# Performance work log

Measured on AMD Instinct MI355X. Metric: run time of the kernel, lower is better.

Reference implementation:

```python
import jax, jax.numpy as jnp
import numpy as np
from jax import lax

B_, L_, D_MODEL = 2, 2048, 1024
H, P, N, G, K, CHUNK = 32, 64, 128, 1, 4, 256
INTER = H * P                 # 2048
CONV_DIM = INTER + 2 * G * N  # 2304
PROJ = INTER + CONV_DIM + H   # 4384: [gate | hidden_B_C | dt]
EPS = 1e-6


def segment_sum(x):
    # x: [..., T] -> [..., T, T]; segsum[i,j] = sum_{k=j+1..i} x[k] for i>=j, else -inf
    T = x.shape[-1]
    xx = jnp.repeat(x[..., None], T, axis=-1)
    xx = jnp.where(jnp.tril(jnp.ones((T, T), bool), -1), xx, 0.0)
    s = jnp.cumsum(xx, axis=-2)
    return jnp.where(jnp.tril(jnp.ones((T, T), bool)), s, -jnp.inf)


def setup_inputs() -> dict:
    key = jax.random.key(0)
    ks = jax.random.split(key, 6)
    s = 0.02
    return {
        "x": jax.random.normal(ks[0], (B_, L_, D_MODEL), jnp.float32),
        "in_proj_w": jax.random.normal(ks[1], (PROJ, D_MODEL), jnp.float32) * s,
        "conv_w": jax.random.normal(ks[2], (CONV_DIM, 1, K), jnp.float32) * s,
        "conv_b": jnp.zeros((CONV_DIM,), jnp.float32),
        "dt_bias": jax.random.uniform(ks[3], (H,), jnp.float32, 0.0, 1.0),
        "A_log": jnp.log(jnp.arange(1, H + 1, dtype=jnp.float32)),
        "D": jnp.ones((H,), jnp.float32),
        "norm_w": jnp.ones((INTER,), jnp.float32),
        "out_proj_w": jax.random.normal(ks[4], (D_MODEL, INTER), jnp.float32) * s,
    }


def _forward(x, in_proj_w, conv_w, conv_b, dt_bias, A_log, D, norm_w, out_proj_w):
    b, L, _ = x.shape
    proj = x @ in_proj_w.T                                    # [b,L,PROJ]
    gate, hBC, dt = jnp.split(proj, [INTER, INTER + CONV_DIM], axis=-1)
    # depthwise causal conv1d over sequence
    xc = jnp.pad(hBC.transpose(0, 2, 1), ((0, 0), (0, 0), (K - 1, 0)))
    conv = lax.conv_general_dilated(xc, conv_w, (1,), 'VALID',
                                    dimension_numbers=('NCH', 'OIH', 'NCH'),
                                    feature_group_count=CONV_DIM)
    hBC = jax.nn.silu((conv + conv_b[None, :, None]).transpose(0, 2, 1))  # [b,L,CONV_DIM]
    hs, Bm, Cm = jnp.split(hBC, [INTER, INTER + G * N], axis=-1)
    hs = hs.reshape(b, L, H, P)
    Bm = jnp.repeat(Bm.reshape(b, L, G, N), H // G, axis=2)   # [b,L,H,N]
    Cm = jnp.repeat(Cm.reshape(b, L, G, N), H // G, axis=2)
    dt = jax.nn.softplus(dt + dt_bias)                        # [b,L,H]
    A = -jnp.exp(A_log)                                       # [H]
    D_res = hs * D[None, None, :, None]
    hs = hs * dt[..., None]
    Adt = dt * A                                              # [b,L,H]
    c = L // CHUNK
    A_c = Adt.reshape(b, c, CHUNK, H).transpose(0, 3, 1, 2)   # [b,H,c,l]
    A_cum = jnp.cumsum(A_c, axis=-1)
    Lmat = jnp.exp(segment_sum(A_c))                          # [b,H,c,l,l]
    hs_c = hs.reshape(b, c, CHUNK, H, P)
    B_c = Bm.reshape(b, c, CHUNK, H, N)
    C_c = Cm.reshape(b, c, CHUNK, H, N)
    # intra-chunk (diagonal blocks)
    Gm = jnp.einsum('bcshn,bczhn->bchsz', C_c, B_c)
    M = Gm * Lmat.transpose(0, 2, 1, 3, 4)
    Y_diag = jnp.einsum('bchsz,bczhp->bcshp', M, hs_c)
    # per-chunk final states
    decay_states = jnp.exp(A_cum[..., -1:] - A_cum)           # [b,H,c,l]
    B_decay = B_c * decay_states.transpose(0, 2, 3, 1)[..., None]
    states = jnp.einsum('bclhn,bclhp->bchpn', B_decay, hs_c)  # [b,c,H,P,N]
    # inter-chunk recurrence
    decay_chunk = jnp.exp(segment_sum(jnp.pad(A_cum[..., -1], ((0, 0), (0, 0), (1, 0)))))  # [b,H,c+1,c+1]
    states0 = jnp.concatenate([jnp.zeros_like(states[:, :1]), states], axis=1)             # [b,c+1,H,P,N]
    prev = jnp.einsum('bhij,bjhpn->bihpn', decay_chunk, states0)[:, :-1]                   # [b,c,H,P,N]
    # off-diagonal contribution
    state_decay = jnp.exp(A_cum).transpose(0, 2, 3, 1)        # [b,c,l,H]
    Y_off = jnp.einsum('bclhn,bchpn->bclhp', C_c, prev) * state_decay[..., None]
    y = ((Y_diag + Y_off).reshape(b, L, H, P) + D_res).reshape(b, L, INTER)
    # gated grouped RMSNorm (group_size = INTER // G)
    gs = INTER // G
    yf = y.astype(jnp.float32) * jax.nn.silu(gate.astype(jnp.float32))
    yg = yf.reshape(b, L, INTER // gs, gs)
    var = jnp.mean(yg * yg, axis=-1, keepdims=True)
    yn = (yg * lax.rsqrt(var + EPS)).reshape(b, L, INTER) * norm_w
    return yn @ out_proj_w.T


def reference(x, in_proj_w, conv_w, conv_b, dt_bias, A_log, D, norm_w, out_proj_w):
    return _forward(x, in_proj_w, conv_w, conv_b, dt_bias, A_log, D, norm_w, out_proj_w)
```

## Files before the change

kernel.cpp:

```cpp
#include <hip/hip_runtime.h>
#include <stdint.h>

typedef __attribute__((ext_vector_type(8))) short short8;
typedef __attribute__((ext_vector_type(4))) float f32x4;

#define DEV static __device__ __forceinline__
#define LOG2E 1.44269504088896340736f

DEV float b2f(unsigned short u) { union { float f; unsigned int i; } x; x.i = ((unsigned int)u) << 16; return x.f; }
DEV unsigned short f2b(float f) {
    union { float f; unsigned int i; } x; x.f = f;
    unsigned int r = x.i + 0x7fffu + ((x.i >> 16) & 1u);
    return (unsigned short)(r >> 16);
}
DEV void gld_lds16(const void* g, void* l) {
    __builtin_amdgcn_global_load_lds((const __attribute__((address_space(1))) void*)g,
                                     (__attribute__((address_space(3))) void*)l, 16, 0, 0);
}
DEV int xcd_swizzle(int bid, int nwg) {
    int q = nwg >> 3, r = nwg & 7;
    int xcd = bid & 7, base = bid >> 3;
    return (xcd < r ? xcd * (q + 1) : r * (q + 1) + (xcd - r) * q) + base;
}

__global__ void cast3_kernel(const float* __restrict__ a, unsigned short* __restrict__ oa, long na8,
                             const float* __restrict__ b, unsigned short* __restrict__ ob_, long nb8,
                             const float* __restrict__ c, unsigned short* __restrict__ oc, long nc8) {
    long i = (long)blockIdx.x * blockDim.x + threadIdx.x;
    long stride = (long)gridDim.x * blockDim.x;
    long tot = na8 + nb8 + nc8;
    for (; i < tot; i += stride) {
        const float* src; unsigned short* dst; long j = i;
        if (j < na8) { src = a; dst = oa; }
        else if (j < na8 + nb8) { j -= na8; src = b; dst = ob_; }
        else { j -= na8 + nb8; src = c; dst = oc; }
        const f32x4* p = (const f32x4*)(src + j * 8);
        f32x4 v0 = p[0], v1 = p[1];
        short8 o;
        o[0] = (short)f2b(v0[0]); o[1] = (short)f2b(v0[1]); o[2] = (short)f2b(v0[2]); o[3] = (short)f2b(v0[3]);
        o[4] = (short)f2b(v1[0]); o[5] = (short)f2b(v1[1]); o[6] = (short)f2b(v1[2]); o[7] = (short)f2b(v1[3]);
        *(short8*)(dst + j * 8) = o;
    }
}

template<int OMODE>
__global__ __launch_bounds__(256) void gemm_nt(
    const unsigned short* __restrict__ A, int lda, long sAy, long sAz,
    const unsigned short* __restrict__ B, int ldb, long sBy, long sBz,
    void* __restrict__ Cp, int ldc, long sCy, long sCz,
    float* __restrict__ aux,
    int M, int N, int K, int tn)
{
    A += (long)blockIdx.y * sAy + (long)blockIdx.z * sAz;
    B += (long)blockIdx.y * sBy + (long)blockIdx.z * sBz;
    int bid = xcd_swizzle(blockIdx.x, gridDim.x);
    int im = bid / tn, in_ = bid % tn;
    int m0 = im * 128, n0 = in_ * 128;
    __shared__ short smem[2 * 2 * 128 * 64];
    int tid = threadIdx.x;
    int lane = tid & 63, wave = tid >> 6;
    int wu = __builtin_amdgcn_readfirstlane(wave);
    int wm = wave >> 1, wn = wave & 1;
    f32x4 acc[4][4];
#pragma unroll
    for (int m = 0; m < 4; m++)
#pragma unroll
        for (int n = 0; n < 4; n++) acc[m][n] = (f32x4){0.f, 0.f, 0.f, 0.f};

    auto stage = [&](int k0, int s) {
        short* As = smem + s * 16384;
        short* Bs = As + 8192;
#pragma unroll
        for (int i = 0; i < 4; ++i) {
            int g = i * 256 + tid;
            int r = g >> 3, pc = g & 7;
            int cc = pc ^ (r & 7);
            gld_lds16(A + (long)(m0 + r) * lda + k0 + cc * 8, As + (i * 256 + wu * 64) * 8);
            int rb = n0 + r; rb = rb < N ? rb : N - 1;
            gld_lds16(B + (long)rb * ldb + k0 + cc * 8, Bs + (i * 256 + wu * 64) * 8);
        }
    };

    int nt = K >> 6;
    stage(0, 0);
    for (int t = 0; t < nt; ++t) {
        int cur = t & 1;
        if (t + 1 < nt) {
            stage((t + 1) << 6, cur ^ 1);
            asm volatile("s_waitcnt vmcnt(8)" ::: "memory");
        } else {
            asm volatile("s_waitcnt vmcnt(0)" ::: "memory");
        }
        __builtin_amdgcn_s_barrier();
        const short* As = smem + cur * 16384;
        const short* Bs = As + 8192;
#pragma unroll
        for (int ks = 0; ks < 2; ++ks) {
            short8 af[4], bfr[4];
#pragma unroll
            for (int m = 0; m < 4; ++m) {
                int r = wm * 64 + m * 16 + (lane & 15);
                int pc = (ks * 4 + (lane >> 4)) ^ (r & 7);
                af[m] = *(const short8*)(As + r * 64 + pc * 8);
            }
#pragma unroll
            for (int n = 0; n < 4; ++n) {
                int r = wn * 64 + n * 16 + (lane & 15);
                int pc = (ks * 4 + (lane >> 4)) ^ (r & 7);
                bfr[n] = *(const short8*)(Bs + r * 64 + pc * 8);
            }
            __builtin_amdgcn_s_setprio(1);
#pragma unroll
            for (int m = 0; m < 4; ++m)
#pragma unroll
                for (int n = 0; n < 4; ++n)
                    acc[m][n] = __builtin_amdgcn_mfma_f32_16x16x32_bf16(af[m], bfr[n], acc[m][n], 0, 0, 0);
            __builtin_amdgcn_s_setprio(0);
        }
        __builtin_amdgcn_s_barrier();
    }

    int rbase = m0 + wm * 64 + ((lane >> 4) << 2);
    int cbase = n0 + wn * 64 + (lane & 15);
    if (OMODE == 0) {
        float* C = (float*)Cp;
        C += (long)blockIdx.y * sCy + (long)blockIdx.z * sCz;
#pragma unroll
        for (int m = 0; m < 4; ++m)
#pragma unroll
            for (int n = 0; n < 4; ++n) {
                int col = cbase + n * 16;
                if (col < N) {
#pragma unroll
                    for (int r = 0; r < 4; ++r)
                        C[(long)(rbase + m * 16 + r) * ldc + col] = acc[m][n][r];
                }
            }
    } else if (OMODE == 4) {
        float* C = (float*)Cp;
#pragma unroll
        for (int m = 0; m < 4; ++m)
#pragma unroll
            for (int r = 0; r < 4; ++r) {
                int row = rbase + m * 16 + r;
                float sc = rsqrtf(aux[row] * (1.f / 2048.f) + 1e-6f);
#pragma unroll
                for (int n = 0; n < 4; ++n)
                    C[(long)row * ldc + cbase + n * 16] = acc[m][n][r] * sc;
            }
    } else if (OMODE == 1) {
        unsigned short* Cs = (unsigned short*)smem;
        int rl = wm * 64 + ((lane >> 4) << 2);
        int cl = wn * 64 + (lane & 15);
#pragma unroll
        for (int m = 0; m < 4; ++m)
#pragma unroll
            for (int r = 0; r < 4; ++r) {
                int row = rl + m * 16 + r;
                int xr = ((row >> 2) & 3) << 4;
#pragma unroll
                for (int n = 0; n < 4; ++n)
                    Cs[row * 128 + ((cl + n * 16) ^ xr)] = f2b(acc[m][n][r]);
            }
        __syncthreads();
        unsigned short* C = (unsigned short*)Cp;
        C += (long)blockIdx.y * sCy + (long)blockIdx.z * sCz;
#pragma unroll
        for (int j = 0; j < 8; ++j) {
            int chunk = j * 256 + tid;
            int row = chunk >> 4, c8 = (chunk & 15) * 8;
            int col = n0 + c8;
            int xr = ((row >> 2) & 3) << 4;
            if (col < N)
                *(short8*)(C + (long)(m0 + row) * ldc + col) = *(const short8*)(Cs + row * 128 + (c8 ^ xr));
        }
    } else {
#pragma unroll
        for (int m = 0; m < 4; ++m)
#pragma unroll
            for (int n = 0; n < 4; ++n) {
                int col = cbase + n * 16;
                if (col >= 4352 && col < N) {
#pragma unroll
                    for (int r = 0; r < 4; ++r)
                        aux[(long)(rbase + m * 16 + r) * 32 + (col - 4352)] = acc[m][n][r];
                }
            }
        unsigned short* T = (unsigned short*)smem;
        int rl = wm * 64 + ((lane >> 4) << 2);
        int cl = wn * 64 + (lane & 15);
#pragma unroll
        for (int n = 0; n < 4; ++n) {
            int ch = cl + n * 16;
            int sw = (ch & 15) << 3;
#pragma unroll
            for (int m = 0; m < 4; ++m)
#pragma unroll
                for (int r = 0; r < 4; ++r) {
                    int mrow = rl + m * 16 + r;
                    T[ch * 128 + (mrow ^ sw)] = f2b(acc[m][n][r]);
                }
        }
        __syncthreads();
        unsigned short* C = (unsigned short*)Cp;
#pragma unroll
        for (int j = 0; j < 8; ++j) {
            int idx = j * 256 + tid;
            int ch = idx >> 4, mc8 = (idx & 15) * 8;
            int gch = n0 + ch;
            if (gch < N) {
                short8 o = *(const short8*)(T + ch * 128 + (mc8 ^ ((ch & 15) << 3)));
                *(short8*)(C + (long)gch * ldc + m0 + mc8) = o;
            }
        }
    }
}

__global__ __launch_bounds__(256) void dtcum_kernel(
    const float* __restrict__ dtraw,
    const float* __restrict__ dt_bias, const float* __restrict__ A_log,
    float* __restrict__ dtv, float* __restrict__ Acum, float* __restrict__ Atot)
{
    int bh = blockIdx.x;
    int b = bh >> 5, h = bh & 31;
    int tid = threadIdx.x;
    float bias = dt_bias[h];
    float negA = -__expf(A_log[h]);
    __shared__ float s[256];
    for (int c = 0; c < 8; ++c) {
        int t = c * 256 + tid;
        float v = dtraw[(long)(b * 2048 + t) * 32 + h] + bias;
        float dt = v > 20.f ? v : log1pf(__expf(v));
        dtv[(long)bh * 2048 + t] = dt;
        s[tid] = dt * negA;
        __syncthreads();
        for (int off = 1; off < 256; off <<= 1) {
            float x = (tid >= off) ? s[tid - off] : 0.f;
            __syncthreads();
            s[tid] += x;
            __syncthreads();
        }
        Acum[(long)bh * 2048 + t] = s[tid];
        if (tid == 255) Atot[bh * 8 + c] = s[255];
        __syncthreads();
    }
}

__global__ __launch_bounds__(256) void convT_kernel(
    const unsigned short* __restrict__ projT,
    const float* __restrict__ conv_w, const float* __restrict__ conv_b,
    const float* __restrict__ dtv, const float* __restrict__ Acum, const float* __restrict__ Atot,
    unsigned short* __restrict__ xdtT, unsigned short* __restrict__ xdtd,
    unsigned short* __restrict__ Bb, unsigned short* __restrict__ Cb, unsigned short* __restrict__ BT)
{
    int tt = blockIdx.x;
    int cht = blockIdx.y;
    int b = blockIdx.z;
    int t0 = tt * 256;
    int ch0 = cht * 64;
    int tid = threadIdx.x;
    __shared__ short raw[64 * 264];
    __shared__ unsigned short trsp[256 * 64];
    __shared__ float sdt[256], sac[256];
    __shared__ float satot;
    bool hidden = cht < 32;
    for (int j = 0; j < 9; ++j) {
        int idx = j * 256 + tid;
        if (idx < 64 * 33) {
            int r = idx / 33, cc = idx % 33;
            int tg = t0 - 8 + cc * 8;
            short8 v = {0, 0, 0, 0, 0, 0, 0, 0};
            if (tg >= 0)
                v = *(const short8*)(projT + (long)(2048 + ch0 + r) * 4096 + b * 2048 + tg);
            *(short8*)(raw + r * 264 + cc * 8) = v;
        }
    }
    if (hidden) {
        int h = cht;
        sdt[tid] = dtv[(long)(b * 32 + h) * 2048 + t0 + tid];
        sac[tid] = Acum[(long)(b * 32 + h) * 2048 + t0 + tid];
        if (tid == 0) satot = Atot[(b * 32 + h) * 8 + tt];
    }
    __syncthreads();
    for (int p = 0; p < 8; ++p) {
        int ch = p * 8 + (tid >> 5);
        int tb = (tid & 31) * 8;
        int cg = ch0 + ch;
        f32x4 wv = *(const f32x4*)(conv_w + cg * 4);
        float cb = conv_b[cg];
        float s[8];
#pragma unroll
        for (int j = 0; j < 8; ++j) {
            int tl = tb + j;
            float a = cb;
#pragma unroll
            for (int k = 0; k < 4; ++k)
                a += b2f((unsigned short)raw[ch * 264 + tl + 5 + k]) * wv[k];
            s[j] = a / (1.f + __expf(-a));
        }
        if (hidden) {
            short8 o1, o2;
#pragma unroll
            for (int j = 0; j < 8; ++j) {
                int tl = tb + j;
                float xdt = s[j] * sdt[tl];
                float dec = __expf(satot - sac[tl]);
                o1[j] = (short)f2b(xdt);
                o2[j] = (short)f2b(xdt * dec);
            }
            long off = (long)cg * 4096 + b * 2048 + t0 + tb;
            *(short8*)(xdtT + off) = o1;
            *(short8*)(xdtd + off) = o2;
        } else {
            short8 o;
#pragma unroll
            for (int j = 0; j < 8; ++j) o[j] = (short)f2b(s[j]);
            if (cht < 34) {
                int n = (cht - 32) * 64 + ch;
                *(short8*)(BT + (long)n * 4096 + b * 2048 + t0 + tb) = o;
            }
#pragma unroll
            for (int j = 0; j < 8; ++j) {
                int tl = tb + j;
                trsp[tl * 64 + (ch ^ ((tl & 7) << 3))] = (unsigned short)o[j];
            }
        }
    }
    if (!hidden) {
        __syncthreads();
        unsigned short* dst = (cht < 34) ? Bb : Cb;
        int n0 = ((cht - 32) & 1) * 64;
        for (int p = 0; p < 8; ++p) {
            int idx = p * 256 + tid;
            int tl = idx >> 3, c8 = (idx & 7) * 8;
            short8 o;
#pragma unroll
            for (int q = 0; q < 8; ++q)
                o[q] = (short)trsp[tl * 64 + ((c8 + q) ^ ((tl & 7) << 3))];
            *(short8*)(dst + (long)(b * 2048 + t0 + tl) * 128 + n0 + c8) = o;
        }
    }
}

__global__ __launch_bounds__(256) void ydiagoff_kernel(
    const unsigned short* __restrict__ Gm,
    const float* __restrict__ Acum,
    const unsigned short* __restrict__ xdtT,
    const unsigned short* __restrict__ projT,
    const unsigned short* __restrict__ Cb,
    const unsigned short* __restrict__ prevb,
    const float* __restrict__ dtv,
    const float* __restrict__ Dp,
    const float* __restrict__ norm_w,
    unsigned short* __restrict__ ynu,
    float* __restrict__ ssq)
{
    int blk = blockIdx.x;
    int h = blk & 31, bc = blk >> 5;
    int c = bc & 7, b = bc >> 3;
    int tid = threadIdx.x, lane = tid & 63, wave = tid >> 6;
    __shared__ float sAc[256];
    __shared__ short Mb[256 * 64];
    __shared__ float sdi[256];
    __shared__ float snw[64];
    __shared__ unsigned short yt[256 * 72];
    float Dv = Dp[h];
    sAc[tid] = Acum[(long)(b * 32 + h) * 2048 + c * 256 + tid] * LOG2E;
    sdi[tid] = Dv / dtv[(long)(b * 32 + h) * 2048 + c * 256 + tid];
    if (tid < 64) snw[tid] = norm_w[h * 64 + tid];
    __syncthreads();
    f32x4 acc[4][4];
#pragma unroll
    for (int m = 0; m < 4; m++)
#pragma unroll
        for (int n = 0; n < 4; n++) acc[m][n] = (f32x4){0.f, 0.f, 0.f, 0.f};

#pragma unroll
    for (int zp = 0; zp < 4; ++zp) {
        const int z0 = zp * 64;
        const int niter = 8 - zp * 2;
        for (int i = 0; i < niter; ++i) {
            int ci = i * 256 + tid;
            int s = z0 + (ci >> 3), cz = ci & 7;
            int zc0 = z0 + cz * 8;
            short8 gv = *(const short8*)(Gm + ((long)bc * 256 + s) * 256 + zc0);
            float as = sAc[s];
            short8 o;
#pragma unroll
            for (int j = 0; j < 8; ++j) {
                int z = zc0 + j;
                float e = (s >= z) ? exp2f(as - sAc[z]) : 0.f;
                float mval = b2f((unsigned short)gv[j]) * e;
                if (s == z) mval += sdi[s];
                o[j] = (short)f2b(mval);
            }
            *(short8*)(Mb + s * 64 + (cz ^ (s & 7)) * 8) = o;
        }
        __syncthreads();
#pragma unroll
        for (int ks = 0; ks < 2; ++ks) {
            short8 af[4], bfr[4];
#pragma unroll
            for (int m = 0; m < 4; ++m) {
                if (wave * 64 + m * 16 >= z0) {
                    int r = wave * 64 + m * 16 + (lane & 15);
                    int pc = (ks * 4 + (lane >> 4)) ^ (r & 7);
                    af[m] = *(const short8*)(Mb + r * 64 + pc * 8);
                }
            }
#pragma unroll
            for (int n = 0; n < 4; ++n) {
                int p = n * 16 + (lane & 15);
                int zcol = c * 256 + z0 + ks * 32 + (lane >> 4) * 8;
                bfr[n] = *(const short8*)(xdtT + (long)(h * 64 + p) * 4096 + b * 2048 + zcol);
            }
#pragma unroll
            for (int m = 0; m < 4; ++m) {
                if (wave * 64 + m * 16 >= z0) {
#pragma unroll
                    for (int n = 0; n < 4; ++n)
                        acc[m][n] = __builtin_amdgcn_mfma_f32_16x16x32_bf16(af[m], bfr[n], acc[m][n], 0, 0, 0);
                }
            }
        }
        __syncthreads();
    }
    float el[4];
#pragma unroll
    for (int m = 0; m < 4; ++m) el[m] = exp2f(sAc[wave * 64 + m * 16 + (lane & 15)]);
#pragma unroll
    for (int ks = 0; ks < 4; ++ks) {
        short8 af[4], bfr[4];
#pragma unroll
        for (int m = 0; m < 4; ++m) {
            int l = wave * 64 + m * 16 + (lane & 15);
            short8 cv = *(const short8*)(Cb + ((long)b * 2048 + c * 256 + l) * 128 + ks * 32 + (lane >> 4) * 8);
#pragma unroll
            for (int j = 0; j < 8; ++j) af[m][j] = (short)f2b(b2f((unsigned short)cv[j]) * el[m]);
        }
#pragma unroll
        for (int n = 0; n < 4; ++n) {
            int p = n * 16 + (lane & 15);
            bfr[n] = *(const short8*)(prevb + ((long)(bc * 32 + h) * 64 + p) * 128 + ks * 32 + (lane >> 4) * 8);
        }
#pragma unroll
        for (int m = 0; m < 4; ++m)
#pragma unroll
            for (int n = 0; n < 4; ++n)
                acc[m][n] = __builtin_amdgcn_mfma_f32_16x16x32_bf16(af[m], bfr[n], acc[m][n], 0, 0, 0);
    }
    unsigned short* gt = (unsigned short*)Mb;
#pragma unroll
    for (int i = 0; i < 8; ++i) {
        int idx = i * 256 + tid;
        int r = idx >> 5, c8 = (idx & 31) * 8;
        short8 v = *(const short8*)(projT + (long)(h * 64 + r) * 4096 + b * 2048 + c * 256 + c8);
#pragma unroll
        for (int j = 0; j < 8; ++j)
            gt[r * 256 + ((c8 + j) ^ ((r & 7) << 3))] = (unsigned short)v[j];
    }
    __syncthreads();
#pragma unroll
    for (int m = 0; m < 4; ++m)
#pragma unroll
        for (int r = 0; r < 4; ++r) {
            int tl = wave * 64 + m * 16 + ((lane >> 4) << 2) + r;
            long bt = (long)b * 2048 + c * 256 + tl;
            float part = 0.f;
#pragma unroll
            for (int n = 0; n < 4; ++n) {
                int cl = n * 16 + (lane & 15);
                float yv = acc[m][n][r];
                float g = b2f(gt[cl * 256 + (tl ^ ((cl & 7) << 3))]);
                float yf = yv * g / (1.f + __expf(-g));
                part += yf * yf;
                yt[tl * 72 + cl] = f2b(yf * snw[cl]);
            }
#pragma unroll
            for (int w2 = 1; w2 < 16; w2 <<= 1) part += __shfl_xor(part, w2);
            if ((lane & 15) == 0) atomicAdd(&ssq[bt], part);
        }
    __syncthreads();
#pragma unroll
    for (int j = 0; j < 8; ++j) {
        int idx = j * 256 + tid;
        int tl = idx >> 3, c8 = (idx & 7) * 8;
        short8 o = *(const short8*)(yt + tl * 72 + c8);
        *(short8*)(ynu + ((long)b * 2048 + c * 256 + tl) * 2048 + h * 64 + c8) = o;
    }
}

__global__ __launch_bounds__(256) void scan_kernel(
    const float* __restrict__ states,
    const float* __restrict__ Atot,
    unsigned short* __restrict__ prevb)
{
    int bh = blockIdx.x;
    int b = bh >> 5, h = bh & 31;
    float ex[8];
#pragma unroll
    for (int c = 0; c < 8; ++c) ex[c] = __expf(Atot[bh * 8 + c]);
    for (int e = threadIdx.x; e < 8192; e += 256) {
        float S = 0.f;
#pragma unroll
        for (int c = 0; c < 8; ++c) {
            long idx = (long)((b * 8 + c) * 32 + h) * 8192 + e;
            prevb[idx] = f2b(S);
            S = ex[c] * S + states[idx];
        }
    }
}

extern "C" void kernel_launch(void* const* d_in, const int* in_sizes, int n_in,
                              void* d_out, int out_size, void* d_ws, size_t ws_size,
                              hipStream_t stream)
{
    const float* x        = (const float*)d_in[0];
    const float* in_proj  = (const float*)d_in[1];
    const float* conv_w   = (const float*)d_in[2];
    const float* conv_b   = (const float*)d_in[3];
    const float* dt_bias  = (const float*)d_in[4];
    const float* A_log    = (const float*)d_in[5];
    const float* Dp       = (const float*)d_in[6];
    const float* norm_w   = (const float*)d_in[7];
    const float* out_proj = (const float*)d_in[8];
    float* out = (float*)d_out;

    char* w = (char*)d_ws;
    auto alloc = [&](size_t bytes) { char* p = w; w += (bytes + 255) & ~(size_t)255; return p; };
    unsigned short* xb    = (unsigned short*)alloc(4096L * 1024 * 2);
    unsigned short* wb    = (unsigned short*)alloc(4384L * 1024 * 2);
    unsigned short* ob    = (unsigned short*)alloc(1024L * 2048 * 2);
    unsigned short* projT = (unsigned short*)alloc(4384L * 4096 * 2);
    float*          dtraw = (float*)        alloc(4096L * 32 * 4);
    float*          dtv   = (float*)        alloc(64L * 2048 * 4);
    float*          Acum  = (float*)        alloc(64L * 2048 * 4);
    float*          Atot  = (float*)        alloc(64L * 8 * 4);
    unsigned short* xdtT  = (unsigned short*)alloc(2048L * 4096 * 2);
    unsigned short* xdtd  = (unsigned short*)alloc(2048L * 4096 * 2);
    unsigned short* Bb    = (unsigned short*)alloc(4096L * 128 * 2);
    unsigned short* Cb    = (unsigned short*)alloc(4096L * 128 * 2);
    unsigned short* BT    = (unsigned short*)alloc(128L * 4096 * 2);
    unsigned short* Gmb   = (unsigned short*)alloc(16L * 256 * 256 * 2);
    float*          states= (float*)        alloc(2L * 8 * 2048 * 128 * 4);
    unsigned short* prevb = (unsigned short*)alloc(2L * 8 * 2048 * 128 * 2);
    unsigned short* ynu   = (unsigned short*)alloc(4096L * 2048 * 2);
    float*          ssq   = (float*)        alloc(4096L * 4);

    hipMemsetAsync(ssq, 0, 4096 * 4, stream);

    cast3_kernel<<<2048, 256, 0, stream>>>(x, xb, 4096L * 1024 / 8,
                                           in_proj, wb, 4384L * 1024 / 8,
                                           out_proj, ob, 1024L * 2048 / 8);

    gemm_nt<3><<<dim3(32 * 35, 1, 1), 256, 0, stream>>>(
        xb, 1024, 0, 0, wb, 1024, 0, 0, projT, 4096, 0, 0, dtraw, 4096, 4384, 1024, 35);

    dtcum_kernel<<<64, 256, 0, stream>>>(dtraw, dt_bias, A_log, dtv, Acum, Atot);

    convT_kernel<<<dim3(8, 36, 2), 256, 0, stream>>>(
        projT, conv_w, conv_b, dtv, Acum, Atot, xdtT, xdtd, Bb, Cb, BT);

    gemm_nt<1><<<dim3(4, 8, 2), 256, 0, stream>>>(
        Cb, 128, 256L * 128, 2048L * 128,
        Bb, 128, 256L * 128, 2048L * 128,
        Gmb, 256, 256L * 256, 8L * 256 * 256, nullptr, 256, 256, 128, 2);

    gemm_nt<0><<<dim3(16, 8, 2), 256, 0, stream>>>(
        xdtd, 4096, 256, 2048,
        BT, 4096, 256, 2048,
        states, 128, 2048L * 128, 8L * 2048 * 128, nullptr, 2048, 128, 256, 1);

    scan_kernel<<<64, 256, 0, stream>>>(states, Atot, prevb);

    ydiagoff_kernel<<<512, 256, 0, stream>>>(Gmb, Acum, xdtT, projT, Cb, prevb,
                                             dtv, Dp, norm_w, ynu, ssq);

    gemm_nt<4><<<dim3(32 * 8, 1, 1), 256, 0, stream>>>(
        ynu, 2048, 0, 0, ob, 2048, 0, 0, out, 1024, 0, 0, ssq, 4096, 1024, 2048, 8);
}
```

Before: 296.3 us.

## Use XCD-aware 2D tile mapping in GEMMs and widen dtcum/scan grids

Replaces the linear XCD swizzle in the GEMM with a 2D block mapping. Each of the 8 XCDs gets a rectangular region of output tiles (4x2 groups), so tiles that share A and B rows stay within one XCD's L2. For the in_proj GEMM this launches 1152 blocks, some of which exit early as padding. It also splits dtcum_kernel across chunks (64 to 512 blocks) and scan_kernel across element slices (64 to 512 blocks) to raise occupancy on those small, latency-bound kernels.

```diff
diff --git a/kernel.cpp b/kernel.cpp
--- a/kernel.cpp
+++ b/kernel.cpp
@@ -16,11 +16,6 @@
 DEV void gld_lds16(const void* g, void* l) {
     __builtin_amdgcn_global_load_lds((const __attribute__((address_space(1))) void*)g,
                                      (__attribute__((address_space(3))) void*)l, 16, 0, 0);
-}
-DEV int xcd_swizzle(int bid, int nwg) {
-    int q = nwg >> 3, r = nwg & 7;
-    int xcd = bid & 7, base = bid >> 3;
-    return (xcd < r ? xcd * (q + 1) : r * (q + 1) + (xcd - r) * q) + base;
 }
 
 __global__ void cast3_kernel(const float* __restrict__ a, unsigned short* __restrict__ oa, long na8,
@@ -49,12 +44,22 @@
     const unsigned short* __restrict__ B, int ldb, long sBy, long sBz,
     void* __restrict__ Cp, int ldc, long sCy, long sCz,
     float* __restrict__ aux,
-    int M, int N, int K, int tn)
+    int M, int N, int K, int tm, int tn, int gr)
 {
+    int im, in_;
+    if (gr > 0) {
+        int gc = 8 / gr;
+        int rows_per = (tm + gr - 1) / gr;
+        int cols_per = (tn + gc - 1) / gc;
+        int xcd = blockIdx.x & 7, idx = blockIdx.x >> 3;
+        im = (xcd / gc) * rows_per + idx % rows_per;
+        in_ = (xcd % gc) * cols_per + idx / rows_per;
+        if (im >= tm || in_ >= tn) return;
+    } else {
+        im = blockIdx.x / tn; in_ = blockIdx.x % tn;
+    }
     A += (long)blockIdx.y * sAy + (long)blockIdx.z * sAz;
     B += (long)blockIdx.y * sBy + (long)blockIdx.z * sBz;
-    int bid = xcd_swizzle(blockIdx.x, gridDim.x);
-    int im = bid / tn, in_ = bid % tn;
     int m0 = im * 128, n0 = in_ * 128;
     __shared__ short smem[2 * 2 * 128 * 64];
     int tid = threadIdx.x;
@@ -221,29 +226,27 @@
     const float* __restrict__ dt_bias, const float* __restrict__ A_log,
     float* __restrict__ dtv, float* __restrict__ Acum, float* __restrict__ Atot)
 {
-    int bh = blockIdx.x;
+    int blk = blockIdx.x;
+    int c = blk & 7, bh = blk >> 3;
     int b = bh >> 5, h = bh & 31;
     int tid = threadIdx.x;
     float bias = dt_bias[h];
     float negA = -__expf(A_log[h]);
     __shared__ float s[256];
-    for (int c = 0; c < 8; ++c) {
-        int t = c * 256 + tid;
-        float v = dtraw[(long)(b * 2048 + t) * 32 + h] + bias;
-        float dt = v > 20.f ? v : log1pf(__expf(v));
-        dtv[(long)bh * 2048 + t] = dt;
-        s[tid] = dt * negA;
-        __syncthreads();
-        for (int off = 1; off < 256; off <<= 1) {
-            float x = (tid >= off) ? s[tid - off] : 0.f;
-            __syncthreads();
-            s[tid] += x;
-            __syncthreads();
-        }
-        Acum[(long)bh * 2048 + t] = s[tid];
-        if (tid == 255) Atot[bh * 8 + c] = s[255];
-        __syncthreads();
-    }
+    int t = c * 256 + tid;
+    float v = dtraw[(long)(b * 2048 + t) * 32 + h] + bias;
+    float dt = v > 20.f ? v : log1pf(__expf(v));
+    dtv[(long)bh * 2048 + t] = dt;
+    s[tid] = dt * negA;
+    __syncthreads();
+    for (int off = 1; off < 256; off <<= 1) {
+        float x = (tid >= off) ? s[tid - off] : 0.f;
+        __syncthreads();
+        s[tid] += x;
+        __syncthreads();
+    }
+    Acum[(long)bh * 2048 + t] = s[tid];
+    if (tid == 255) Atot[bh * 8 + c] = s[255];
 }
 
 __global__ __launch_bounds__(256) void convT_kernel(
@@ -495,12 +498,14 @@
     const float* __restrict__ Atot,
     unsigned short* __restrict__ prevb)
 {
-    int bh = blockIdx.x;
+    int blk = blockIdx.x;
+    int bh = blk >> 3, slice = blk & 7;
     int b = bh >> 5, h = bh & 31;
     float ex[8];
 #pragma unroll
     for (int c = 0; c < 8; ++c) ex[c] = __expf(Atot[bh * 8 + c]);
-    for (int e = threadIdx.x; e < 8192; e += 256) {
+    int e0 = slice * 1024;
+    for (int e = e0 + threadIdx.x; e < e0 + 1024; e += 256) {
         float S = 0.f;
 #pragma unroll
         for (int c = 0; c < 8; ++c) {
@@ -553,10 +558,11 @@
                                            in_proj, wb, 4384L * 1024 / 8,
                                            out_proj, ob, 1024L * 2048 / 8);
 
-    gemm_nt<3><<<dim3(32 * 35, 1, 1), 256, 0, stream>>>(
-        xb, 1024, 0, 0, wb, 1024, 0, 0, projT, 4096, 0, 0, dtraw, 4096, 4384, 1024, 35);
-
-    dtcum_kernel<<<64, 256, 0, stream>>>(dtraw, dt_bias, A_log, dtv, Acum, Atot);
+    gemm_nt<3><<<dim3(1152, 1, 1), 256, 0, stream>>>(
+        xb, 1024, 0, 0, wb, 1024, 0, 0, projT, 4096, 0, 0, dtraw,
+        4096, 4384, 1024, 32, 35, 4);
+
+    dtcum_kernel<<<512, 256, 0, stream>>>(dtraw, dt_bias, A_log, dtv, Acum, Atot);
 
     convT_kernel<<<dim3(8, 36, 2), 256, 0, stream>>>(
         projT, conv_w, conv_b, dtv, Acum, Atot, xdtT, xdtd, Bb, Cb, BT);
@@ -564,18 +570,21 @@
     gemm_nt<1><<<dim3(4, 8, 2), 256, 0, stream>>>(
         Cb, 128, 256L * 128, 2048L * 128,
         Bb, 128, 256L * 128, 2048L * 128,
-        Gmb, 256, 256L * 256, 8L * 256 * 256, nullptr, 256, 256, 128, 2);
+        Gmb, 256, 256L * 256, 8L * 256 * 256, nullptr,
+        256, 256, 128, 2, 2, 0);
 
     gemm_nt<0><<<dim3(16, 8, 2), 256, 0, stream>>>(
         xdtd, 4096, 256, 2048,
         BT, 4096, 256, 2048,
-        states, 128, 2048L * 128, 8L * 2048 * 128, nullptr, 2048, 128, 256, 1);
-
-    scan_kernel<<<64, 256, 0, stream>>>(states, Atot, prevb);
+        states, 128, 2048L * 128, 8L * 2048 * 128, nullptr,
+        2048, 128, 256, 16, 1, 0);
+
+    scan_kernel<<<512, 256, 0, stream>>>(states, Atot, prevb);
 
     ydiagoff_kernel<<<512, 256, 0, stream>>>(Gmb, Acum, xdtT, projT, Cb, prevb,
                                              dtv, Dp, norm_w, ynu, ssq);
 
-    gemm_nt<4><<<dim3(32 * 8, 1, 1), 256, 0, stream>>>(
-        ynu, 2048, 0, 0, ob, 2048, 0, 0, out, 1024, 0, 0, ssq, 4096, 1024, 2048, 8);
-}
+    gemm_nt<4><<<dim3(256, 1, 1), 256, 0, stream>>>(
+        ynu, 2048, 0, 0, ob, 2048, 0, 0, out, 1024, 0, 0, ssq,
+        4096, 1024, 2048, 32, 8, 4);
+}
```

New measurement: 273.4 us. -7.7%, faster.
